# Optimization experiments

Hardware: AMD Instinct MI355X
Metric: run time of the kernel (lower is better)

## Reference

```python
import jax, jax.numpy as jnp
import numpy as np

RATIO = 0.25
RADIUS = 0.2
NSAMPLE = 32


def fps(xyz, S):
    """Farthest point sampling. xyz: [B,N,3] -> indices [B,S] (int32)."""
    B, N, _ = xyz.shape

    def step(carry, _):
        min_d, last_idx = carry  # [B,N], [B]
        centroid = jnp.take_along_axis(xyz, last_idx[:, None, None], axis=1)  # [B,1,3]
        d = jnp.sum((xyz - centroid) ** 2, axis=-1)  # [B,N]
        min_d = jnp.minimum(min_d, d)
        nxt = jnp.argmax(min_d, axis=-1).astype(jnp.int32)
        return (min_d, nxt), last_idx

    init = (jnp.full((B, N), 1e10, xyz.dtype), jnp.zeros((B,), jnp.int32))
    _, idxs = jax.lax.scan(step, init, None, length=S)  # [S,B]
    return idxs.T  # [B,S]


def ball_query(radius, nsample, xyz, new_xyz):
    """xyz: [B,N,3], new_xyz: [B,S,3] -> group idx [B,S,nsample] (int32)."""
    B, S, _ = new_xyz.shape
    N = xyz.shape[1]
    sqd = jnp.sum((new_xyz[:, :, None, :] - xyz[:, None, :, :]) ** 2, axis=-1)  # [B,S,N]
    idx = jnp.broadcast_to(jnp.arange(N, dtype=jnp.int32), (B, S, N))
    idx = jnp.where(sqd > radius * radius, N, idx)
    idx = jnp.sort(idx, axis=-1)[:, :, :nsample]  # first nsample in-ball ids (ascending)
    first = idx[:, :, :1]
    idx = jnp.where(idx == N, first, idx)  # pad empties with first neighbor
    return idx


def reference(xyz, features, W1, b1, W2, b2):
    B, N, _ = xyz.shape
    S = int(N * RATIO)
    fps_idx = fps(xyz, S)  # [B,S]
    new_xyz = jnp.take_along_axis(xyz, fps_idx[:, :, None], axis=1)  # [B,S,3]
    grp_idx = ball_query(RADIUS, NSAMPLE, xyz, new_xyz)  # [B,S,K]
    batch = jnp.arange(B, dtype=jnp.int32)[:, None, None]
    new_points = features[batch, grp_idx]  # [B,S,K,D]
    # shared MLP (1x1 Conv2d equivalents) + ReLU
    h = jax.nn.relu(jnp.einsum('bskd,ed->bske', new_points, W1) + b1)
    h = jax.nn.relu(jnp.einsum('bskd,ed->bske', h, W2) + b2)
    new_points_out = jnp.max(h, axis=2)  # max over group K -> [B,S,D']
    new_points_out = new_points_out.transpose(0, 2, 1)  # [B,D',S]
    new_xyz_out = new_xyz.transpose(0, 2, 1)  # [B,3,S]
    return new_xyz_out, new_points_out


def setup_inputs() -> dict:
    key = jax.random.key(0)
    k1, k2, k3, k4 = jax.random.split(key, 4)
    B, N, D = 16, 4096, 64
    xyz = jax.random.uniform(k1, (B, N, 3), dtype=jnp.float32)
    features = jax.random.normal(k2, (B, N, D), dtype=jnp.float32)
    W1 = jax.random.normal(k3, (64, 64), dtype=jnp.float32) * (1.0 / np.sqrt(64))
    b1 = jnp.zeros((64,), jnp.float32)
    W2 = jax.random.normal(k4, (128, 64), dtype=jnp.float32) * (1.0 / np.sqrt(64))
    b2 = jnp.zeros((128,), jnp.float32)
    return {"xyz": xyz, "features": features, "W1": W1, "b1": b1, "W2": W2, "b2": b2}
```

## Files before the change

kernel.cpp:

```cpp
#include <hip/hip_runtime.h>
#include <hip/hip_bf16.h>

#define BATCH 16
#define NPTS  4096
#define NSAMP 1024
#define KNB   32
#define DFEAT 64

#define THREADS  512
#define FPS_PPT  (NPTS / THREADS)
#define NWV      (THREADS / 64)
#define NWBLK    240
#define NWAVES   (NWBLK * NWV)
#define NTASK    (BATCH * NSAMP)
#define TAG_BASE 0xC0FFEE00u

template <int CTRL, int RMASK>
__device__ __forceinline__ void dpp_round(unsigned long long& key) {
    const int klo = (int)(unsigned)key;
    const int khi = (int)(unsigned)(key >> 32);
    const int tlo = __builtin_amdgcn_update_dpp(klo, klo, CTRL, RMASK, 0xF, false);
    const int thi = __builtin_amdgcn_update_dpp(khi, khi, CTRL, RMASK, 0xF, false);
    const unsigned long long tk =
        ((unsigned long long)(unsigned)thi << 32) | (unsigned)tlo;
    if (tk > key) key = tk;
}

__device__ __forceinline__ void pub_store(unsigned long long* p, unsigned long long v) {
    __hip_atomic_store(p, v, __ATOMIC_RELAXED, __HIP_MEMORY_SCOPE_AGENT);
}
__device__ __forceinline__ unsigned long long pub_load(const unsigned long long* p) {
    return __hip_atomic_load(p, __ATOMIC_RELAXED, __HIP_MEMORY_SCOPE_AGENT);
}

__device__ __forceinline__ void barrier_lds_only() {
    asm volatile("s_waitcnt lgkmcnt(0)" ::: "memory");
    __builtin_amdgcn_s_barrier();
}

__global__ __launch_bounds__(THREADS) void fused_kernel(
    const float* __restrict__ xyz, const float* __restrict__ features,
    const float* __restrict__ W1, const float* __restrict__ b1,
    const float* __restrict__ W2, const float* __restrict__ b2,
    float* __restrict__ out_xyz, float* __restrict__ out_pts,
    unsigned long long* __restrict__ pub) {

    __shared__ alignas(16) unsigned char smem[65536 + 12288 + 128];
    const int bid  = blockIdx.x;
    const int tid  = threadIdx.x;
    const int lane = tid & 63;
    const int wid  = tid >> 6;

    if (bid < BATCH) {
        float4* sc = (float4*)smem;
        float* stX = (float*)(smem + 65536);
        float* stY = stX + NSAMP;
        float* stZ = stY + NSAMP;
        unsigned long long* pw = (unsigned long long*)(smem + 65536 + 12288);

        float px[FPS_PPT], py[FPS_PPT], pz[FPS_PPT], md[FPS_PPT];
        const float* base = xyz + (size_t)bid * NPTS * 3;
#pragma unroll
        for (int j = 0; j < FPS_PPT; j++) {
            const int i = j * THREADS + tid;
            const float x = base[i * 3 + 0];
            const float y = base[i * 3 + 1];
            const float z = base[i * 3 + 2];
            sc[i] = make_float4(x, y, z, 0.0f);
            px[j] = x; py[j] = y; pz[j] = z;
            md[j] = 1e10f;
        }

        float cx = base[0], cy = base[1], cz = base[2];
        unsigned long long* pb = pub + (size_t)bid * NSAMP * 3;
        if (tid == 0) {
            stX[0] = cx; stY[0] = cy; stZ[0] = cz;
            pub_store(&pb[0], ((unsigned long long)__float_as_uint(cx) << 32) | (TAG_BASE + 0));
            pub_store(&pb[1], ((unsigned long long)__float_as_uint(cy) << 32) | (TAG_BASE + 0));
            pub_store(&pb[2], ((unsigned long long)__float_as_uint(cz) << 32) | (TAG_BASE + 0));
        }
        __syncthreads();

        for (int s = 1; s < NSAMP; s++) {
            float best = -1.0f;
            int   bj   = 0;
#pragma unroll
            for (int j = 0; j < FPS_PPT; j++) {
                const float dx = px[j] - cx;
                const float dy = py[j] - cy;
                const float dz = pz[j] - cz;
                const float d = __fadd_rn(__fadd_rn(__fmul_rn(dx, dx), __fmul_rn(dy, dy)),
                                          __fmul_rn(dz, dz));
                const float m = fminf(md[j], d);
                md[j] = m;
                if (m > best) { best = m; bj = j; }
            }
            const int bi = (bj << 9) | tid;
            unsigned long long key =
                ((unsigned long long)__float_as_uint(best) << 32) | (unsigned)(~bi);
            dpp_round<0x111, 0xF>(key);
            dpp_round<0x112, 0xF>(key);
            dpp_round<0x114, 0xF>(key);
            dpp_round<0x118, 0xF>(key);
            dpp_round<0x142, 0xA>(key);
            dpp_round<0x143, 0xC>(key);

            const int par = s & 1;
            if (lane == 63) pw[par * NWV + wid] = key;
            barrier_lds_only();
            const ulong2 p01 = *(const ulong2*)&pw[par * NWV + 0];
            const ulong2 p23 = *(const ulong2*)&pw[par * NWV + 2];
            const ulong2 p45 = *(const ulong2*)&pw[par * NWV + 4];
            const ulong2 p67 = *(const ulong2*)&pw[par * NWV + 6];
            unsigned long long t0 = p01.x > p01.y ? p01.x : p01.y;
            unsigned long long t1 = p23.x > p23.y ? p23.x : p23.y;
            unsigned long long t2 = p45.x > p45.y ? p45.x : p45.y;
            unsigned long long t3 = p67.x > p67.y ? p67.x : p67.y;
            t0 = t0 > t1 ? t0 : t1;
            t2 = t2 > t3 ? t2 : t3;
            const unsigned long long bk = t0 > t2 ? t0 : t2;
            const int bix = (int)(~(unsigned)bk);

            const float4 c = sc[bix];
            cx = c.x; cy = c.y; cz = c.z;
            if (tid == 0) {
                stX[s] = cx; stY[s] = cy; stZ[s] = cz;
            }
            if ((s & 3) == 0) {
                if (wid == 1 && lane < 12) {
                    const int st   = s - 4 + (lane / 3);
                    const int comp = lane - (lane / 3) * 3;
                    const float v  = comp == 0 ? stX[st] : (comp == 1 ? stY[st] : stZ[st]);
                    pub_store(&pb[3 * st + comp],
                              ((unsigned long long)__float_as_uint(v) << 32) |
                              (TAG_BASE + (unsigned)st));
                }
            }
        }

        __syncthreads();
        if (tid < 12) {
            const int st   = (NSAMP - 4) + (tid / 3);
            const int comp = tid - (tid / 3) * 3;
            const float v  = comp == 0 ? stX[st] : (comp == 1 ? stY[st] : stZ[st]);
            pub_store(&pb[3 * st + comp],
                      ((unsigned long long)__float_as_uint(v) << 32) |
                      (TAG_BASE + (unsigned)st));
        }
        float* ob = out_xyz + (size_t)bid * 3 * NSAMP;
        for (int i = tid; i < NSAMP; i += THREADS) {
            ob[0 * NSAMP + i] = stX[i];
            ob[1 * NSAMP + i] = stY[i];
            ob[2 * NSAMP + i] = stZ[i];
        }
    } else {
        float (*xls)[KNB][DFEAT] = (float (*)[KNB][DFEAT])smem;
        float (*h1s)[DFEAT]      = (float (*)[DFEAT])(smem + 65536);
        int   (*gl)[KNB]         = (int (*)[KNB])(smem + 65536 + 2048);

        float w1r[64], w2ra[64], w2rb[64];
        {
            const float4* W1v = (const float4*)(W1 + (size_t)lane * 64);
            const float4* W2a = (const float4*)(W2 + (size_t)lane * 64);
            const float4* W2b = (const float4*)(W2 + (size_t)(lane + 64) * 64);
#pragma unroll
            for (int i = 0; i < 16; i++) {
                float4 v = W1v[i];
                w1r[4 * i] = v.x; w1r[4 * i + 1] = v.y; w1r[4 * i + 2] = v.z; w1r[4 * i + 3] = v.w;
                v = W2a[i];
                w2ra[4 * i] = v.x; w2ra[4 * i + 1] = v.y; w2ra[4 * i + 2] = v.z; w2ra[4 * i + 3] = v.w;
                v = W2b[i];
                w2rb[4 * i] = v.x; w2rb[4 * i + 1] = v.y; w2rb[4 * i + 2] = v.z; w2rb[4 * i + 3] = v.w;
            }
        }
        const float b1r  = b1[lane];
        const float b2ra = b2[lane];
        const float b2rb = b2[lane + 64];

        const int gwave = (bid - BATCH) * NWV + wid;
        for (int t = gwave; t < NTASK; t += NWAVES) {
            const int sq = t >> 4;
            const int b  = t & 15;

            const unsigned long long* pp = pub + ((size_t)b * NSAMP + sq) * 3;
            const unsigned exp_tag = TAG_BASE + sq;
            float pxf = 0.0f, pyf = 0.0f, pzf = 0.0f;
            if (lane == 0) {
                unsigned long long w0, w1, w2;
                for (;;) {
                    w0 = pub_load(&pp[0]);
                    w1 = pub_load(&pp[1]);
                    w2 = pub_load(&pp[2]);
                    if ((unsigned)w0 == exp_tag && (unsigned)w1 == exp_tag &&
                        (unsigned)w2 == exp_tag) break;
                    __builtin_amdgcn_s_sleep(2);
                }
                pxf = __uint_as_float((unsigned)(w0 >> 32));
                pyf = __uint_as_float((unsigned)(w1 >> 32));
                pzf = __uint_as_float((unsigned)(w2 >> 32));
            }
            const float cx = __shfl(pxf, 0);
            const float cy = __shfl(pyf, 0);
            const float cz = __shfl(pzf, 0);

            const float* base = xyz + (size_t)b * NPTS * 3;
            const float r2 = 0.04f;
            int cnt = 0;
            int firstCand = 0x7fffffff;
            for (int bp = 0; bp < NPTS && cnt < KNB; bp += 64) {
                const int p = bp + lane;
                const float dx = base[p * 3 + 0] - cx;
                const float dy = base[p * 3 + 1] - cy;
                const float dz = base[p * 3 + 2] - cz;
                const float d = __fadd_rn(__fadd_rn(__fmul_rn(dx, dx), __fmul_rn(dy, dy)),
                                          __fmul_rn(dz, dz));
                const bool ok = !(d > r2);
                const unsigned long long m = __ballot(ok);
                const int rank = cnt + (int)__popcll(m & ((1ull << lane) - 1ull));
                if (ok && rank < KNB) gl[wid][rank] = p;
                if (ok && rank == 0) firstCand = p;
                cnt += (int)__popcll(m);
            }
            const int found = cnt < KNB ? cnt : KNB;
            if (found < KNB) {
#pragma unroll
                for (int off = 32; off > 0; off >>= 1) {
                    const int o = __shfl_xor(firstCand, off);
                    firstCand = o < firstCand ? o : firstCand;
                }
                for (int r = found + lane; r < KNB; r += 64) gl[wid][r] = firstCand;
            }
            int gi = 0;
            if (lane < KNB) gi = gl[wid][lane];

            const float* fb = features + (size_t)b * NPTS * DFEAT;
            for (int k = 0; k < KNB; k++) {
                const int idxk = __shfl(gi, k);
                xls[wid][k][lane] = fb[(size_t)idxk * DFEAT + lane];
            }

            float m0 = 0.0f, m1 = 0.0f;
            for (int k = 0; k < KNB; k++) {
                float acc = b1r;
                const float4* xk = (const float4*)xls[wid][k];
#pragma unroll
                for (int i = 0; i < 16; i++) {
                    const float4 v = xk[i];
                    acc = fmaf(v.x, w1r[4 * i], acc);
                    acc = fmaf(v.y, w1r[4 * i + 1], acc);
                    acc = fmaf(v.z, w1r[4 * i + 2], acc);
                    acc = fmaf(v.w, w1r[4 * i + 3], acc);
                }
                h1s[wid][lane] = fmaxf(acc, 0.0f);
                float a0 = b2ra, a1 = b2rb;
                const float4* hv4 = (const float4*)h1s[wid];
#pragma unroll
                for (int i = 0; i < 16; i++) {
                    const float4 v = hv4[i];
                    a0 = fmaf(v.x, w2ra[4 * i], a0);
                    a0 = fmaf(v.y, w2ra[4 * i + 1], a0);
                    a0 = fmaf(v.z, w2ra[4 * i + 2], a0);
                    a0 = fmaf(v.w, w2ra[4 * i + 3], a0);
                    a1 = fmaf(v.x, w2rb[4 * i], a1);
                    a1 = fmaf(v.y, w2rb[4 * i + 1], a1);
                    a1 = fmaf(v.z, w2rb[4 * i + 2], a1);
                    a1 = fmaf(v.w, w2rb[4 * i + 3], a1);
                }
                m0 = fmaxf(m0, fmaxf(a0, 0.0f));
                m1 = fmaxf(m1, fmaxf(a1, 0.0f));
            }

            out_pts[(size_t)b * 128 * NSAMP + (size_t)lane * NSAMP + sq]        = m0;
            out_pts[(size_t)b * 128 * NSAMP + (size_t)(lane + 64) * NSAMP + sq] = m1;
        }
    }
}

extern "C" void kernel_launch(void* const* d_in, const int* in_sizes, int n_in,
                              void* d_out, int out_size, void* d_ws, size_t ws_size,
                              hipStream_t stream) {
    const float* xyz      = (const float*)d_in[0];
    const float* features = (const float*)d_in[1];
    const float* W1       = (const float*)d_in[2];
    const float* b1       = (const float*)d_in[3];
    const float* W2       = (const float*)d_in[4];
    const float* b2       = (const float*)d_in[5];

    float* out_xyz = (float*)d_out;
    float* out_pts = (float*)d_out + (size_t)BATCH * 3 * NSAMP;

    unsigned long long* pub = (unsigned long long*)d_ws;

    fused_kernel<<<BATCH + NWBLK, THREADS, 0, stream>>>(
        xyz, features, W1, b1, W2, b2, out_xyz, out_pts, pub);
}
```

Baseline: 704.3 us.

## Process two batches per FPS block and publish centroids every step

Each farthest-point-sampling block now runs two batch elements interleaved, so the two independent serial chains can hide each other's latency, and fewer blocks are devoted to FPS. Sampled centroids are published to the consumer waves every step instead of in groups of four, which cuts consumer wait latency. The cost is doubled per-step work and register state per FPS thread. Shared memory also grows to about 152 KB, which limits every block to one per CU.

```diff
diff --git a/kernel.cpp b/kernel.cpp
--- a/kernel.cpp
+++ b/kernel.cpp
@@ -10,10 +10,22 @@
 #define THREADS  512
 #define FPS_PPT  (NPTS / THREADS)
 #define NWV      (THREADS / 64)
-#define NWBLK    240
+#define NFPSB    8
+#define NWBLK    248
 #define NWAVES   (NWBLK * NWV)
 #define NTASK    (BATCH * NSAMP)
 #define TAG_BASE 0xC0FFEE00u
+
+#define SCA_OFF  0
+#define SCB_OFF  65536
+#define STAX_OFF 131072
+#define STAY_OFF 135168
+#define STAZ_OFF 139264
+#define STBX_OFF 143360
+#define STBY_OFF 147456
+#define STBZ_OFF 151552
+#define PW_OFF   155648
+#define SMEM_SZ  155904
 
 template <int CTRL, int RMASK>
 __device__ __forceinline__ void dpp_round(unsigned long long& key) {
@@ -38,6 +50,20 @@
     __builtin_amdgcn_s_barrier();
 }
 
+__device__ __forceinline__ unsigned long long combine8(const unsigned long long* p) {
+    const ulong2 p01 = *(const ulong2*)&p[0];
+    const ulong2 p23 = *(const ulong2*)&p[2];
+    const ulong2 p45 = *(const ulong2*)&p[4];
+    const ulong2 p67 = *(const ulong2*)&p[6];
+    unsigned long long t0 = p01.x > p01.y ? p01.x : p01.y;
+    unsigned long long t1 = p23.x > p23.y ? p23.x : p23.y;
+    unsigned long long t2 = p45.x > p45.y ? p45.x : p45.y;
+    unsigned long long t3 = p67.x > p67.y ? p67.x : p67.y;
+    t0 = t0 > t1 ? t0 : t1;
+    t2 = t2 > t3 ? t2 : t3;
+    return t0 > t2 ? t0 : t2;
+}
+
 __global__ __launch_bounds__(THREADS) void fused_kernel(
     const float* __restrict__ xyz, const float* __restrict__ features,
     const float* __restrict__ W1, const float* __restrict__ b1,
@@ -45,113 +71,132 @@
     float* __restrict__ out_xyz, float* __restrict__ out_pts,
     unsigned long long* __restrict__ pub) {
 
-    __shared__ alignas(16) unsigned char smem[65536 + 12288 + 128];
+    __shared__ alignas(16) unsigned char smem[SMEM_SZ];
     const int bid  = blockIdx.x;
     const int tid  = threadIdx.x;
     const int lane = tid & 63;
     const int wid  = tid >> 6;
 
-    if (bid < BATCH) {
-        float4* sc = (float4*)smem;
-        float* stX = (float*)(smem + 65536);
-        float* stY = stX + NSAMP;
-        float* stZ = stY + NSAMP;
-        unsigned long long* pw = (unsigned long long*)(smem + 65536 + 12288);
-
-        float px[FPS_PPT], py[FPS_PPT], pz[FPS_PPT], md[FPS_PPT];
-        const float* base = xyz + (size_t)bid * NPTS * 3;
+    if (bid < NFPSB) {
+        const int bA = 2 * bid, bB = 2 * bid + 1;
+        float4* scA = (float4*)(smem + SCA_OFF);
+        float4* scB = (float4*)(smem + SCB_OFF);
+        float* stAX = (float*)(smem + STAX_OFF);
+        float* stAY = (float*)(smem + STAY_OFF);
+        float* stAZ = (float*)(smem + STAZ_OFF);
+        float* stBX = (float*)(smem + STBX_OFF);
+        float* stBY = (float*)(smem + STBY_OFF);
+        float* stBZ = (float*)(smem + STBZ_OFF);
+        unsigned long long* pwb = (unsigned long long*)(smem + PW_OFF);
+
+        float pxA[FPS_PPT], pyA[FPS_PPT], pzA[FPS_PPT], mdA[FPS_PPT];
+        float pxB[FPS_PPT], pyB[FPS_PPT], pzB[FPS_PPT], mdB[FPS_PPT];
+        const float* baseA = xyz + (size_t)bA * NPTS * 3;
+        const float* baseB = xyz + (size_t)bB * NPTS * 3;
 #pragma unroll
         for (int j = 0; j < FPS_PPT; j++) {
             const int i = j * THREADS + tid;
-            const float x = base[i * 3 + 0];
-            const float y = base[i * 3 + 1];
-            const float z = base[i * 3 + 2];
-            sc[i] = make_float4(x, y, z, 0.0f);
-            px[j] = x; py[j] = y; pz[j] = z;
-            md[j] = 1e10f;
-        }
-
-        float cx = base[0], cy = base[1], cz = base[2];
-        unsigned long long* pb = pub + (size_t)bid * NSAMP * 3;
+            float x = baseA[i * 3 + 0], y = baseA[i * 3 + 1], z = baseA[i * 3 + 2];
+            scA[i] = make_float4(x, y, z, 0.0f);
+            pxA[j] = x; pyA[j] = y; pzA[j] = z; mdA[j] = 1e10f;
+            x = baseB[i * 3 + 0]; y = baseB[i * 3 + 1]; z = baseB[i * 3 + 2];
+            scB[i] = make_float4(x, y, z, 0.0f);
+            pxB[j] = x; pyB[j] = y; pzB[j] = z; mdB[j] = 1e10f;
+        }
+
+        float cxA = baseA[0], cyA = baseA[1], czA = baseA[2];
+        float cxB = baseB[0], cyB = baseB[1], czB = baseB[2];
+        unsigned long long* pbA = pub + (size_t)bA * NSAMP * 3;
+        unsigned long long* pbB = pub + (size_t)bB * NSAMP * 3;
         if (tid == 0) {
-            stX[0] = cx; stY[0] = cy; stZ[0] = cz;
-            pub_store(&pb[0], ((unsigned long long)__float_as_uint(cx) << 32) | (TAG_BASE + 0));
-            pub_store(&pb[1], ((unsigned long long)__float_as_uint(cy) << 32) | (TAG_BASE + 0));
-            pub_store(&pb[2], ((unsigned long long)__float_as_uint(cz) << 32) | (TAG_BASE + 0));
+            stAX[0] = cxA; stAY[0] = cyA; stAZ[0] = czA;
+            stBX[0] = cxB; stBY[0] = cyB; stBZ[0] = czB;
+            pub_store(&pbA[0], ((unsigned long long)__float_as_uint(cxA) << 32) | (TAG_BASE + 0));
+            pub_store(&pbA[1], ((unsigned long long)__float_as_uint(cyA) << 32) | (TAG_BASE + 0));
+            pub_store(&pbA[2], ((unsigned long long)__float_as_uint(czA) << 32) | (TAG_BASE + 0));
+            pub_store(&pbB[0], ((unsigned long long)__float_as_uint(cxB) << 32) | (TAG_BASE + 0));
+            pub_store(&pbB[1], ((unsigned long long)__float_as_uint(cyB) << 32) | (TAG_BASE + 0));
+            pub_store(&pbB[2], ((unsigned long long)__float_as_uint(czB) << 32) | (TAG_BASE + 0));
         }
         __syncthreads();
 
         for (int s = 1; s < NSAMP; s++) {
-            float best = -1.0f;
-            int   bj   = 0;
+            float bestA = -1.0f; int bjA = 0;
 #pragma unroll
             for (int j = 0; j < FPS_PPT; j++) {
-                const float dx = px[j] - cx;
-                const float dy = py[j] - cy;
-                const float dz = pz[j] - cz;
+                const float dx = pxA[j] - cxA;
+                const float dy = pyA[j] - cyA;
+                const float dz = pzA[j] - czA;
                 const float d = __fadd_rn(__fadd_rn(__fmul_rn(dx, dx), __fmul_rn(dy, dy)),
                                           __fmul_rn(dz, dz));
-                const float m = fminf(md[j], d);
-                md[j] = m;
-                if (m > best) { best = m; bj = j; }
-            }
-            const int bi = (bj << 9) | tid;
-            unsigned long long key =
-                ((unsigned long long)__float_as_uint(best) << 32) | (unsigned)(~bi);
-            dpp_round<0x111, 0xF>(key);
-            dpp_round<0x112, 0xF>(key);
-            dpp_round<0x114, 0xF>(key);
-            dpp_round<0x118, 0xF>(key);
-            dpp_round<0x142, 0xA>(key);
-            dpp_round<0x143, 0xC>(key);
+                const float m = fminf(mdA[j], d);
+                mdA[j] = m;
+                if (m > bestA) { bestA = m; bjA = j; }
+            }
+            float bestB = -1.0f; int bjB = 0;
+#pragma unroll
+            for (int j = 0; j < FPS_PPT; j++) {
+                const float dx = pxB[j] - cxB;
+                const float dy = pyB[j] - cyB;
+                const float dz = pzB[j] - czB;
+                const float d = __fadd_rn(__fadd_rn(__fmul_rn(dx, dx), __fmul_rn(dy, dy)),
+                                          __fmul_rn(dz, dz));
+                const float m = fminf(mdB[j], d);
+                mdB[j] = m;
+                if (m > bestB) { bestB = m; bjB = j; }
+            }
+            const int biA = (bjA << 9) | tid;
+            const int biB = (bjB << 9) | tid;
+            unsigned long long keyA =
+                ((unsigned long long)__float_as_uint(bestA) << 32) | (unsigned)(~biA);
+            unsigned long long keyB =
+                ((unsigned long long)__float_as_uint(bestB) << 32) | (unsigned)(~biB);
+            dpp_round<0x111, 0xF>(keyA); dpp_round<0x111, 0xF>(keyB);
+            dpp_round<0x112, 0xF>(keyA); dpp_round<0x112, 0xF>(keyB);
+            dpp_round<0x114, 0xF>(keyA); dpp_round<0x114, 0xF>(keyB);
+            dpp_round<0x118, 0xF>(keyA); dpp_round<0x118, 0xF>(keyB);
+            dpp_round<0x142, 0xA>(keyA); dpp_round<0x142, 0xA>(keyB);
+            dpp_round<0x143, 0xC>(keyA); dpp_round<0x143, 0xC>(keyB);
 
             const int par = s & 1;
-            if (lane == 63) pw[par * NWV + wid] = key;
+            if (lane == 63) {
+                pwb[par * 16 + wid]     = keyA;
+                pwb[par * 16 + 8 + wid] = keyB;
+            }
             barrier_lds_only();
-            const ulong2 p01 = *(const ulong2*)&pw[par * NWV + 0];
-            const ulong2 p23 = *(const ulong2*)&pw[par * NWV + 2];
-            const ulong2 p45 = *(const ulong2*)&pw[par * NWV + 4];
-            const ulong2 p67 = *(const ulong2*)&pw[par * NWV + 6];
-            unsigned long long t0 = p01.x > p01.y ? p01.x : p01.y;
-            unsigned long long t1 = p23.x > p23.y ? p23.x : p23.y;
-            unsigned long long t2 = p45.x > p45.y ? p45.x : p45.y;
-            unsigned long long t3 = p67.x > p67.y ? p67.x : p67.y;
-            t0 = t0 > t1 ? t0 : t1;
-            t2 = t2 > t3 ? t2 : t3;
-            const unsigned long long bk = t0 > t2 ? t0 : t2;
-            const int bix = (int)(~(unsigned)bk);
-
-            const float4 c = sc[bix];
-            cx = c.x; cy = c.y; cz = c.z;
+            const unsigned long long bkA = combine8(&pwb[par * 16]);
+            const unsigned long long bkB = combine8(&pwb[par * 16 + 8]);
+            const int bixA = (int)(~(unsigned)bkA);
+            const int bixB = (int)(~(unsigned)bkB);
+
+            const float4 cA = scA[bixA];
+            const float4 cB = scB[bixB];
+            cxA = cA.x; cyA = cA.y; czA = cA.z;
+            cxB = cB.x; cyB = cB.y; czB = cB.z;
             if (tid == 0) {
-                stX[s] = cx; stY[s] = cy; stZ[s] = cz;
-            }
-            if ((s & 3) == 0) {
-                if (wid == 1 && lane < 12) {
-                    const int st   = s - 4 + (lane / 3);
-                    const int comp = lane - (lane / 3) * 3;
-                    const float v  = comp == 0 ? stX[st] : (comp == 1 ? stY[st] : stZ[st]);
-                    pub_store(&pb[3 * st + comp],
-                              ((unsigned long long)__float_as_uint(v) << 32) |
-                              (TAG_BASE + (unsigned)st));
-                }
+                stAX[s] = cxA; stAY[s] = cyA; stAZ[s] = czA;
+                pub_store(&pbA[3 * s + 0], ((unsigned long long)__float_as_uint(cxA) << 32) | (TAG_BASE + s));
+                pub_store(&pbA[3 * s + 1], ((unsigned long long)__float_as_uint(cyA) << 32) | (TAG_BASE + s));
+                pub_store(&pbA[3 * s + 2], ((unsigned long long)__float_as_uint(czA) << 32) | (TAG_BASE + s));
+            }
+            if (tid == 64) {
+                stBX[s] = cxB; stBY[s] = cyB; stBZ[s] = czB;
+                pub_store(&pbB[3 * s + 0], ((unsigned long long)__float_as_uint(cxB) << 32) | (TAG_BASE + s));
+                pub_store(&pbB[3 * s + 1], ((unsigned long long)__float_as_uint(cyB) << 32) | (TAG_BASE + s));
+                pub_store(&pbB[3 * s + 2], ((unsigned long long)__float_as_uint(czB) << 32) | (TAG_BASE + s));
             }
         }
 
         __syncthreads();
-        if (tid < 12) {
-            const int st   = (NSAMP - 4) + (tid / 3);
-            const int comp = tid - (tid / 3) * 3;
-            const float v  = comp == 0 ? stX[st] : (comp == 1 ? stY[st] : stZ[st]);
-            pub_store(&pb[3 * st + comp],
-                      ((unsigned long long)__float_as_uint(v) << 32) |
-                      (TAG_BASE + (unsigned)st));
-        }
-        float* ob = out_xyz + (size_t)bid * 3 * NSAMP;
+        float* obA = out_xyz + (size_t)bA * 3 * NSAMP;
+        float* obB = out_xyz + (size_t)bB * 3 * NSAMP;
         for (int i = tid; i < NSAMP; i += THREADS) {
-            ob[0 * NSAMP + i] = stX[i];
-            ob[1 * NSAMP + i] = stY[i];
-            ob[2 * NSAMP + i] = stZ[i];
+            obA[0 * NSAMP + i] = stAX[i];
+            obA[1 * NSAMP + i] = stAY[i];
+            obA[2 * NSAMP + i] = stAZ[i];
+            obB[0 * NSAMP + i] = stBX[i];
+            obB[1 * NSAMP + i] = stBY[i];
+            obB[2 * NSAMP + i] = stBZ[i];
         }
     } else {
         float (*xls)[KNB][DFEAT] = (float (*)[KNB][DFEAT])smem;
@@ -177,7 +222,7 @@
         const float b2ra = b2[lane];
         const float b2rb = b2[lane + 64];
 
-        const int gwave = (bid - BATCH) * NWV + wid;
+        const int gwave = (bid - NFPSB) * NWV + wid;
         for (int t = gwave; t < NTASK; t += NWAVES) {
             const int sq = t >> 4;
             const int b  = t & 15;
@@ -291,6 +336,6 @@
 
     unsigned long long* pub = (unsigned long long*)d_ws;
 
-    fused_kernel<<<BATCH + NWBLK, THREADS, 0, stream>>>(
+    fused_kernel<<<NFPSB + NWBLK, THREADS, 0, stream>>>(
         xyz, features, W1, b1, W2, b2, out_xyz, out_pts, pub);
 }
```

New measurement: 1.249 ms. 1.77x slower.
